# Kernel tuning notes

Measured on AMD Instinct MI355X. Metric: run time of the kernel, lower is better.

Reference implementation:

```python
import jax, jax.numpy as jnp
import numpy as np

T, B, IN, H, A = 512, 256, 292, 128, 12


def setup_inputs() -> dict:
    key = jax.random.key(0)
    ks = jax.random.split(key, 8)
    s = 1.0 / np.sqrt(H)
    return {
        "x": jax.random.normal(ks[0], (T, B, IN), dtype=jnp.float32),
        "done": jax.random.randint(ks[1], (T, B), 0, 2, dtype=jnp.int32),
        "h0": jax.random.normal(ks[2], (1, B, H), dtype=jnp.float32),
        "c0": jax.random.normal(ks[3], (1, B, H), dtype=jnp.float32),
        "W_ih": jax.random.normal(ks[4], (4 * H, IN), dtype=jnp.float32) * s,
        "W_hh": jax.random.normal(ks[5], (4 * H, H), dtype=jnp.float32) * s,
        "b_ih": jnp.zeros((4 * H,), dtype=jnp.float32),
        "b_hh": jnp.zeros((4 * H,), dtype=jnp.float32),
        "W_pi": jax.random.normal(ks[6], (A, H), dtype=jnp.float32) * 0.01,
        "b_pi": jnp.zeros((A,), dtype=jnp.float32),
        "W_v": jax.random.normal(ks[7], (1, H), dtype=jnp.float32),
        "b_v": jnp.zeros((1,), dtype=jnp.float32),
    }


def reference(x, done, h0, c0, W_ih, W_hh, b_ih, b_hh, W_pi, b_pi, W_v, b_v):
    # get_states: per-timestep LSTM with done-based reset of (h, c), as a scan.
    done_f = done.astype(x.dtype)  # [T, B]
    bias = b_ih + b_hh  # [4H]

    def step(carry, inp):
        h, c = carry  # [B, H] each
        x_t, d_t = inp  # [B, IN], [B]
        m = (1.0 - d_t)[:, None]  # reset mask
        h = h * m
        c = c * m
        # PyTorch LSTM gate order: input, forget, cell(g), output
        gates = x_t @ W_ih.T + h @ W_hh.T + bias  # [B, 4H]
        i, f, g, o = jnp.split(gates, 4, axis=-1)
        c = jax.nn.sigmoid(f) * c + jax.nn.sigmoid(i) * jnp.tanh(g)
        h = jax.nn.sigmoid(o) * jnp.tanh(c)
        return (h, c), h

    (hN, cN), hs = jax.lax.scan(step, (h0[0], c0[0]), (x, done_f))
    hidden = hs.reshape(T * B, H)  # flatten(cat(new_hidden), 0, 1)
    logits = hidden @ W_pi.T + b_pi  # policy_layers
    value = hidden @ W_v.T + b_v  # value_layers
    return jnp.concatenate([logits, value], axis=-1)  # [T*B, A+1]
```

## Files before the change

### kernel.cpp

```cpp
#include <hip/hip_runtime.h>
#include <stdint.h>
#include <stddef.h>

#define T_ 512
#define B_ 256
#define IN_ 292
#define H_ 128
#define G4_ 512
#define TB_ 131072
#define LCH 32
#define NCH 16
#define KP_ 320

typedef short bf16x8 __attribute__((ext_vector_type(8)));
typedef float f32x4 __attribute__((ext_vector_type(4)));
typedef unsigned int u32t;

__device__ __forceinline__ unsigned short f2bf(float f) {
  unsigned u = __float_as_uint(f);
  u += 0x7FFFu + ((u >> 16) & 1u);
  return (unsigned short)(u >> 16);
}
__device__ __forceinline__ float bf2f(unsigned short s) {
  return __uint_as_float(((unsigned)s) << 16);
}
__device__ __forceinline__ unsigned bfpack2(float a, float b) {
  unsigned ua = __float_as_uint(a) + 0x8000u;
  unsigned ub = __float_as_uint(b) + 0x8000u;
  return __builtin_amdgcn_perm(ub, ua, 0x07060302u);
}
__device__ __forceinline__ float sigf(float x) {
  return __builtin_amdgcn_rcpf(1.0f + __expf(-x));
}
__device__ __forceinline__ float tanhf_(float x) {
  return 1.0f - 2.0f * __builtin_amdgcn_rcpf(__expf(2.0f * x) + 1.0f);
}
__device__ __forceinline__ void barrier_lds() {
  asm volatile("s_waitcnt lgkmcnt(0)\n\ts_barrier" ::: "memory");
}
__device__ __forceinline__ void gload_lds16(const void* g, void* l) {
  __builtin_amdgcn_global_load_lds(
      (const __attribute__((address_space(1))) u32t*)g,
      (__attribute__((address_space(3))) u32t*)l, 16, 0, 0);
}
__device__ __forceinline__ void load_pr(const unsigned short* p, ushort4* pr) {
  union { uint4 v; ushort4 s[2]; } a, b;
  a.v = *(const uint4*)p;
  b.v = *(const uint4*)(p + 8);
  pr[0] = a.s[0]; pr[1] = a.s[1]; pr[2] = b.s[0]; pr[3] = b.s[1];
}

__global__ __launch_bounds__(256) void k0w_cvt(
    const float* __restrict__ Wih, const float* __restrict__ bih,
    const float* __restrict__ bhh, unsigned short* __restrict__ Wb,
    float* __restrict__ bias2) {
  const int g = blockIdx.x * 256 + threadIdx.x;
  const int jj = g / 40, s = g % 40;
  const int src = (jj & 3) * 128 + (jj >> 2);
  if (g < 512) {
    const int sb = (g & 3) * 128 + (g >> 2);
    bias2[g] = bih[sb] + bhh[sb];
  }
  float4 a = {0.f, 0.f, 0.f, 0.f}, b = {0.f, 0.f, 0.f, 0.f};
  const float* p = Wih + (size_t)src * IN_ + 8 * s;
  if (s < 36) { a = *(const float4*)p; b = *(const float4*)(p + 4); }
  else if (s == 36) { a = *(const float4*)p; }
  uint4 o;
  o.x = bfpack2(a.x, a.y); o.y = bfpack2(a.z, a.w);
  o.z = bfpack2(b.x, b.y); o.w = bfpack2(b.z, b.w);
  *(uint4*)&Wb[(size_t)jj * KP_ + 8 * s] = o;
}

__global__ __launch_bounds__(512, 2) void k1_pregemm(
    const float* __restrict__ x, const unsigned short* __restrict__ Wb,
    const float* __restrict__ bias2, unsigned short* __restrict__ pre2) {
  __shared__ float xr[3][128 * 32];
  __shared__ float xtail[128 * 4];

  const int m0 = blockIdx.x * 128;
  const int tid = threadIdx.x;
  const int w = tid >> 6;
  const int lane = tid & 63;
  const int l15 = lane & 15;
  const int q = lane >> 4;

  if (tid < 128) {
    float4 t = *(const float4*)(x + (size_t)(m0 + tid) * IN_ + 288);
    *(float4*)&xtail[tid * 4] = t;
  }

  bf16x8 af_c[4], af_n[4];
#pragma unroll
  for (int s = 0; s < 4; s++) {
    af_c[s] = *(const bf16x8*)&Wb[(size_t)(w * 64 + 16 * s + l15) * KP_ + q * 8];
    af_n[s] = *(const bf16x8*)&Wb[(size_t)(w * 64 + 16 * s + l15) * KP_ + 32 + q * 8];
  }

#define DMA_TILE(tile)                                                        \
  {                                                                           \
    const int _buf = (tile) % 3;                                              \
    _Pragma("unroll")                                                         \
    for (int _j = 0; _j < 2; _j++) {                                          \
      const int _c = lane + 64 * _j;                                          \
      const int _row = 16 * w + (_c >> 3);                                    \
      const int _slot = _c & 7;                                               \
      const float* _src = x + (size_t)(m0 + _row) * IN_ + (tile) * 32 +       \
                          ((_slot ^ (_row & 7)) * 4);                         \
      gload_lds16(_src, &xr[_buf][w * 512 + _c * 4]);                         \
    }                                                                         \
  }

  f32x4 acc[4][8];
#pragma unroll
  for (int s = 0; s < 4; s++)
#pragma unroll
    for (int ms = 0; ms < 8; ms++) acc[s][ms] = (f32x4){0.f, 0.f, 0.f, 0.f};

  DMA_TILE(0)
  DMA_TILE(1)
  asm volatile("s_waitcnt vmcnt(0) lgkmcnt(0)\n\ts_barrier" ::: "memory");

#pragma unroll
  for (int it = 0; it < 9; it++) {
    const int buf = it % 3;
    bf16x8 bfr[8];
#pragma unroll
    for (int ms = 0; ms < 8; ms++) {
      const int row = 16 * ms + l15;
      const int s0 = (2 * q) ^ (l15 & 7);
      const int s1 = (2 * q + 1) ^ (l15 & 7);
      float4 a = *(const float4*)&xr[buf][row * 32 + s0 * 4];
      float4 b = *(const float4*)&xr[buf][row * 32 + s1 * 4];
      uint4 v;
      v.x = bfpack2(a.x, a.y); v.y = bfpack2(a.z, a.w);
      v.z = bfpack2(b.x, b.y); v.w = bfpack2(b.z, b.w);
      bfr[ms] = *(bf16x8*)&v;
    }
#pragma unroll
    for (int s = 0; s < 4; s++)
#pragma unroll
      for (int ms = 0; ms < 8; ms++)
        acc[s][ms] = __builtin_amdgcn_mfma_f32_16x16x32_bf16(
            af_c[s], bfr[ms], acc[s][ms], 0, 0, 0);
#pragma unroll
    for (int s = 0; s < 4; s++) af_c[s] = af_n[s];
    if (it < 8) {
      const int kk = 32 * (it + 2);
#pragma unroll
      for (int s = 0; s < 4; s++)
        af_n[s] = *(const bf16x8*)&Wb[(size_t)(w * 64 + 16 * s + l15) * KP_ + kk + q * 8];
    }
    if (it < 7) DMA_TILE(it + 2)
    if (it < 7)
      asm volatile("s_waitcnt vmcnt(6) lgkmcnt(0)\n\ts_barrier" ::: "memory");
    else if (it == 7)
      asm volatile("s_waitcnt vmcnt(4) lgkmcnt(0)\n\ts_barrier" ::: "memory");
    else
      asm volatile("s_waitcnt lgkmcnt(0)\n\ts_barrier" ::: "memory");
  }

  {
    bf16x8 bfr[8];
#pragma unroll
    for (int ms = 0; ms < 8; ms++) {
      uint4 v = {0u, 0u, 0u, 0u};
      if (q == 0) {
        float4 t = *(const float4*)&xtail[(16 * ms + l15) * 4];
        v.x = bfpack2(t.x, t.y);
        v.y = bfpack2(t.z, t.w);
      }
      bfr[ms] = *(bf16x8*)&v;
    }
#pragma unroll
    for (int s = 0; s < 4; s++)
#pragma unroll
      for (int ms = 0; ms < 8; ms++)
        acc[s][ms] = __builtin_amdgcn_mfma_f32_16x16x32_bf16(
            af_c[s], bfr[ms], acc[s][ms], 0, 0, 0);
  }

  float4 bb[4];
#pragma unroll
  for (int s = 0; s < 4; s++) bb[s] = *(const float4*)&bias2[w * 64 + 16 * s + 4 * q];
#pragma unroll
  for (int ms = 0; ms < 8; ms++) {
    const int m = m0 + 16 * ms + l15;
#pragma unroll
    for (int s = 0; s < 4; s++) {
      const int jjb = w * 64 + 16 * s + 4 * q;
      uint2 st;
      st.x = bfpack2(acc[s][ms][0] + bb[s].x, acc[s][ms][1] + bb[s].y);
      st.y = bfpack2(acc[s][ms][2] + bb[s].z, acc[s][ms][3] + bb[s].w);
      *(uint2*)&pre2[((size_t)m << 9) + jjb] = st;
    }
  }
#undef DMA_TILE
}

__global__ __launch_bounds__(512) void k2a_chunk(
    const unsigned short* __restrict__ pre2, const float* __restrict__ Whh,
    const int* __restrict__ done, unsigned short* __restrict__ hidden,
    unsigned short* __restrict__ hfin, float* __restrict__ cfin) {
  __shared__ unsigned short hs[2][16 * 136];
  __shared__ int dns[LCH * 16];

  const int bg = blockIdx.x & 15;
  const int ck = blockIdx.x >> 4;
  const int t0 = ck * LCH;
  const int tid = threadIdx.x;
  const int w = tid >> 6;
  const int lane = tid & 63;
  const int l15 = lane & 15;
  const int q = lane >> 4;
  const int bglob = bg * 16 + l15;
  const int kcell = 16 * w + 4 * q;
  const int kq16 = kcell * 4;

  {
    const int r = tid >> 4, c = tid & 15;
    dns[tid] = done[(size_t)(t0 + r) * B_ + bg * 16 + c];
  }

  bf16x8 wf[4][4];
#pragma unroll
  for (int tI = 0; tI < 4; tI++) {
    const int jg = 16 * (w + 8 * tI) + l15;
#pragma unroll
    for (int kc = 0; kc < 4; kc++) {
      const float* p = Whh + (size_t)jg * H_ + kc * 32 + q * 8;
      float4 u0 = *(const float4*)p;
      float4 u1 = *(const float4*)(p + 4);
      bf16x8 r;
      r[0]=(short)f2bf(u0.x); r[1]=(short)f2bf(u0.y); r[2]=(short)f2bf(u0.z); r[3]=(short)f2bf(u0.w);
      r[4]=(short)f2bf(u1.x); r[5]=(short)f2bf(u1.y); r[6]=(short)f2bf(u1.z); r[7]=(short)f2bf(u1.w);
      wf[tI][kc] = r;
    }
  }

  float c_[4] = {0.f, 0.f, 0.f, 0.f};
  {
    const int b = tid >> 5, k = (tid & 31) * 4;
    *(ushort4*)&hs[0][b * 136 + k] = (ushort4){0, 0, 0, 0};
  }
  bool vld = false;
  __syncthreads();

  ushort4 pr[4], prn[4];
  load_pr(pre2 + ((size_t)t0 * B_ + bglob) * G4_ + kq16, pr);
  load_pr(pre2 + ((size_t)(t0 + 1) * B_ + bglob) * G4_ + kq16, prn);

  ushort4 hw = {0, 0, 0, 0};
#pragma unroll 1
  for (int u = 0; u < LCH; u++) {
    const int t = t0 + u;
    ushort4 pr2[4];
    const int un = (u + 2 < LCH) ? u + 2 : LCH - 1;
    load_pr(pre2 + ((size_t)(t0 + un) * B_ + bglob) * G4_ + kq16, pr2);

    const int dn = dns[u * 16 + l15];
    vld = vld || (dn != 0);

    const unsigned short* hb = hs[u & 1];
    bf16x8 hf[4];
#pragma unroll
    for (int kc = 0; kc < 4; kc++) {
      bf16x8 v = *(const bf16x8*)&hb[l15 * 136 + kc * 32 + q * 8];
      if (dn) v = (bf16x8){0, 0, 0, 0, 0, 0, 0, 0};
      hf[kc] = v;
    }

    f32x4 acc[4];
#pragma unroll
    for (int tI = 0; tI < 4; tI++) acc[tI] = (f32x4){0.f, 0.f, 0.f, 0.f};
#pragma unroll
    for (int tI = 0; tI < 4; tI++)
#pragma unroll
      for (int kc = 0; kc < 4; kc++)
        acc[tI] = __builtin_amdgcn_mfma_f32_16x16x32_bf16(
            wf[tI][kc], hf[kc], acc[tI], 0, 0, 0);

    const float m = dn ? 0.0f : 1.0f;
    float hv[4];
#pragma unroll
    for (int r = 0; r < 4; r++) {
      const float iv = acc[0][r] + bf2f(pr[r].x);
      const float fv = acc[1][r] + bf2f(pr[r].y);
      const float gv = acc[2][r] + bf2f(pr[r].z);
      const float ov = acc[3][r] + bf2f(pr[r].w);
      float cc = c_[r] * m;
      cc = sigf(fv) * cc + sigf(iv) * tanhf_(gv);
      c_[r] = cc;
      hv[r] = sigf(ov) * tanhf_(cc);
    }
    uint2 hp = {bfpack2(hv[0], hv[1]), bfpack2(hv[2], hv[3])};
    hw = *(ushort4*)&hp;
    *(uint2*)&hs[(u + 1) & 1][l15 * 136 + kcell] = hp;
    if (vld)
      *(uint2*)&hidden[((size_t)t * B_ + bglob) * H_ + kcell] = hp;
#pragma unroll
    for (int tI = 0; tI < 4; tI++) { pr[tI] = prn[tI]; prn[tI] = pr2[tI]; }
    barrier_lds();
  }

  *(ushort4*)&hfin[((size_t)ck * B_ + bglob) * H_ + kcell] = hw;
  float4 cv = {c_[0], c_[1], c_[2], c_[3]};
  *(float4*)&cfin[((size_t)ck * B_ + bglob) * H_ + kcell] = cv;
}

__global__ __launch_bounds__(512) void k2b_par(
    const unsigned short* __restrict__ pre2, const float* __restrict__ Whh,
    const float* __restrict__ h0, const float* __restrict__ c0,
    const int* __restrict__ done, unsigned short* __restrict__ hidden,
    const unsigned short* __restrict__ hfin, const float* __restrict__ cfin,
    int* __restrict__ needfix) {
  __shared__ unsigned short hs[2][16 * 136];
  __shared__ int dns[LCH * 16];

  const int bg = blockIdx.x & 15;
  const int ck = blockIdx.x >> 4;
  const int t0 = ck * LCH;
  const int tid = threadIdx.x;
  const int w = tid >> 6;
  const int lane = tid & 63;
  const int l15 = lane & 15;
  const int q = lane >> 4;
  const int bglob = bg * 16 + l15;
  const int kcell = 16 * w + 4 * q;
  const int kq16 = kcell * 4;

  {
    const int r = tid >> 4, c = tid & 15;
    dns[tid] = done[(size_t)(t0 + r) * B_ + bg * 16 + c];
  }

  bf16x8 wf[4][4];
#pragma unroll
  for (int tI = 0; tI < 4; tI++) {
    const int jg = 16 * (w + 8 * tI) + l15;
#pragma unroll
    for (int kc = 0; kc < 4; kc++) {
      const float* p = Whh + (size_t)jg * H_ + kc * 32 + q * 8;
      float4 u0 = *(const float4*)p;
      float4 u1 = *(const float4*)(p + 4);
      bf16x8 r;
      r[0]=(short)f2bf(u0.x); r[1]=(short)f2bf(u0.y); r[2]=(short)f2bf(u0.z); r[3]=(short)f2bf(u0.w);
      r[4]=(short)f2bf(u1.x); r[5]=(short)f2bf(u1.y); r[6]=(short)f2bf(u1.z); r[7]=(short)f2bf(u1.w);
      wf[tI][kc] = r;
    }
  }

  float c_[4];
  {
    const int b = tid >> 5, k = (tid & 31) * 4;
    if (ck == 0) {
      float4 hv = *(const float4*)(h0 + (size_t)(bg * 16 + b) * H_ + k);
      uint2 hp = {bfpack2(hv.x, hv.y), bfpack2(hv.z, hv.w)};
      *(uint2*)&hs[0][b * 136 + k] = hp;
      float4 cv = *(const float4*)(c0 + (size_t)bglob * H_ + kcell);
      c_[0] = cv.x; c_[1] = cv.y; c_[2] = cv.z; c_[3] = cv.w;
    } else {
      ushort4 hv = *(const ushort4*)&hfin[((size_t)(ck - 1) * B_ + bg * 16 + b) * H_ + k];
      *(ushort4*)&hs[0][b * 136 + k] = hv;
      float4 cv = *(const float4*)&cfin[((size_t)(ck - 1) * B_ + bglob) * H_ + kcell];
      c_[0] = cv.x; c_[1] = cv.y; c_[2] = cv.z; c_[3] = cv.w;
    }
  }
  int cur = 0;
  bool act = true;
  __syncthreads();

  ushort4 pr[4];
  load_pr(pre2 + ((size_t)t0 * B_ + bglob) * G4_ + kq16, pr);

#pragma unroll 1
  for (int u = 0; u < LCH; u++) {
    const int t = t0 + u;
    const int dn = dns[u * 16 + l15];
    const bool nact = act && (dn == 0);
    if (__ballot(nact) == 0ULL) { act = false; break; }
    act = nact;

    ushort4 prn[4];
    const int un = (u + 1 < LCH) ? u + 1 : LCH - 1;
    load_pr(pre2 + ((size_t)(t0 + un) * B_ + bglob) * G4_ + kq16, prn);

    const unsigned short* hb = hs[cur];
    bf16x8 hf[4];
#pragma unroll
    for (int kc = 0; kc < 4; kc++)
      hf[kc] = *(const bf16x8*)&hb[l15 * 136 + kc * 32 + q * 8];

    f32x4 acc[4];
#pragma unroll
    for (int tI = 0; tI < 4; tI++) acc[tI] = (f32x4){0.f, 0.f, 0.f, 0.f};
#pragma unroll
    for (int tI = 0; tI < 4; tI++)
#pragma unroll
      for (int kc = 0; kc < 4; kc++)
        acc[tI] = __builtin_amdgcn_mfma_f32_16x16x32_bf16(
            wf[tI][kc], hf[kc], acc[tI], 0, 0, 0);

    float hv[4];
#pragma unroll
    for (int r = 0; r < 4; r++) {
      const float iv = acc[0][r] + bf2f(pr[r].x);
      const float fv = acc[1][r] + bf2f(pr[r].y);
      const float gv = acc[2][r] + bf2f(pr[r].z);
      const float ov = acc[3][r] + bf2f(pr[r].w);
      float cc = sigf(fv) * c_[r] + sigf(iv) * tanhf_(gv);
      c_[r] = cc;
      hv[r] = sigf(ov) * tanhf_(cc);
    }
    uint2 hp = {bfpack2(hv[0], hv[1]), bfpack2(hv[2], hv[3])};
    *(uint2*)&hs[cur ^ 1][l15 * 136 + kcell] = hp;
    if (act)
      *(uint2*)&hidden[((size_t)t * B_ + bglob) * H_ + kcell] = hp;
#pragma unroll
    for (int tI = 0; tI < 4; tI++) pr[tI] = prn[tI];
    barrier_lds();
    cur ^= 1;
  }

  if (tid == 0) needfix[blockIdx.x] = (__ballot(act) != 0ULL) ? 1 : 0;
}

__global__ __launch_bounds__(512) void k2c_guard(
    const unsigned short* __restrict__ pre2, const float* __restrict__ Whh,
    const float* __restrict__ h0, const float* __restrict__ c0,
    const int* __restrict__ done, unsigned short* __restrict__ hidden,
    const unsigned short* __restrict__ hfin, const float* __restrict__ cfin,
    const int* __restrict__ needfix) {
  const int bg = blockIdx.x;
  bool dirty = false;
  for (int c2 = 0; c2 < NCH - 1; c2++) dirty |= (needfix[c2 * 16 + bg] != 0);
  if (!dirty) return;

  __shared__ unsigned short hs[2][16 * 136];
  __shared__ int dns[T_ * 16];

  const int tid = threadIdx.x;
  const int w = tid >> 6;
  const int lane = tid & 63;
  const int l15 = lane & 15;
  const int q = lane >> 4;
  const int bglob = bg * 16 + l15;
  const int kcell = 16 * w + 4 * q;
  const int kq16 = kcell * 4;

  {
    const int* p = done + (size_t)tid * B_ + bg * 16;
    *(int4*)&dns[tid * 16]      = *(const int4*)(p);
    *(int4*)&dns[tid * 16 + 4]  = *(const int4*)(p + 4);
    *(int4*)&dns[tid * 16 + 8]  = *(const int4*)(p + 8);
    *(int4*)&dns[tid * 16 + 12] = *(const int4*)(p + 12);
  }

  bf16x8 wf[4][4];
#pragma unroll
  for (int tI = 0; tI < 4; tI++) {
    const int jg = 16 * (w + 8 * tI) + l15;
#pragma unroll
    for (int kc = 0; kc < 4; kc++) {
      const float* p = Whh + (size_t)jg * H_ + kc * 32 + q * 8;
      float4 u0 = *(const float4*)p;
      float4 u1 = *(const float4*)(p + 4);
      bf16x8 r;
      r[0]=(short)f2bf(u0.x); r[1]=(short)f2bf(u0.y); r[2]=(short)f2bf(u0.z); r[3]=(short)f2bf(u0.w);
      r[4]=(short)f2bf(u1.x); r[5]=(short)f2bf(u1.y); r[6]=(short)f2bf(u1.z); r[7]=(short)f2bf(u1.w);
      wf[tI][kc] = r;
    }
  }

  float c_[4];
  {
    float4 cv = *(const float4*)(c0 + (size_t)bglob * H_ + kcell);
    c_[0] = cv.x; c_[1] = cv.y; c_[2] = cv.z; c_[3] = cv.w;
    const int b = tid >> 5, k = (tid & 31) * 4;
    float4 hv = *(const float4*)(h0 + (size_t)(bg * 16 + b) * H_ + k);
    uint2 hp = {bfpack2(hv.x, hv.y), bfpack2(hv.z, hv.w)};
    *(uint2*)&hs[0][b * 136 + k] = hp;
  }
  int cur = 0;
  __syncthreads();

#pragma unroll 1
  for (int ck = 0; ck < NCH; ck++) {
    const int t0 = ck * LCH;
    bool act = true;

    ushort4 pr[4];
    load_pr(pre2 + ((size_t)t0 * B_ + bglob) * G4_ + kq16, pr);

#pragma unroll 1
    for (int u = 0; u < LCH; u++) {
      const int t = t0 + u;
      const int dn = dns[t * 16 + l15];
      const bool nact = act && (dn == 0);
      if (__ballot(nact) == 0ULL) { act = false; break; }
      act = nact;

      ushort4 prn[4];
      const int un = (u + 1 < LCH) ? u + 1 : LCH - 1;
      load_pr(pre2 + ((size_t)(t0 + un) * B_ + bglob) * G4_ + kq16, prn);

      const unsigned short* hb = hs[cur];
      bf16x8 hf[4];
#pragma unroll
      for (int kc = 0; kc < 4; kc++)
        hf[kc] = *(const bf16x8*)&hb[l15 * 136 + kc * 32 + q * 8];

      f32x4 acc[4];
#pragma unroll
      for (int tI = 0; tI < 4; tI++) acc[tI] = (f32x4){0.f, 0.f, 0.f, 0.f};
#pragma unroll
      for (int tI = 0; tI < 4; tI++)
#pragma unroll
        for (int kc = 0; kc < 4; kc++)
          acc[tI] = __builtin_amdgcn_mfma_f32_16x16x32_bf16(
              wf[tI][kc], hf[kc], acc[tI], 0, 0, 0);

      float hv[4];
#pragma unroll
      for (int r = 0; r < 4; r++) {
        const float iv = acc[0][r] + bf2f(pr[r].x);
        const float fv = acc[1][r] + bf2f(pr[r].y);
        const float gv = acc[2][r] + bf2f(pr[r].z);
        const float ov = acc[3][r] + bf2f(pr[r].w);
        float cc = sigf(fv) * c_[r] + sigf(iv) * tanhf_(gv);
        c_[r] = cc;
        hv[r] = sigf(ov) * tanhf_(cc);
      }
      uint2 hp = {bfpack2(hv[0], hv[1]), bfpack2(hv[2], hv[3])};
      *(uint2*)&hs[cur ^ 1][l15 * 136 + kcell] = hp;
      if (act)
        *(uint2*)&hidden[((size_t)t * B_ + bglob) * H_ + kcell] = hp;
#pragma unroll
      for (int tI = 0; tI < 4; tI++) pr[tI] = prn[tI];
      barrier_lds();
      cur ^= 1;
    }

    if (!act) {
      ushort4 hv = *(const ushort4*)&hfin[((size_t)ck * B_ + bglob) * H_ + kcell];
      float4 cv = *(const float4*)&cfin[((size_t)ck * B_ + bglob) * H_ + kcell];
      c_[0] = cv.x; c_[1] = cv.y; c_[2] = cv.z; c_[3] = cv.w;
      *(ushort4*)&hs[cur][l15 * 136 + kcell] = hv;
    }
    barrier_lds();
  }
}

__global__ __launch_bounds__(256) void k3_head(
    const unsigned short* __restrict__ hidden, const float* __restrict__ Wpi,
    const float* __restrict__ bpi, const float* __restrict__ Wv,
    const float* __restrict__ bv, float* __restrict__ out) {
  __shared__ unsigned short hs3[64 * 136];
  __shared__ float bias_s[16];

  const int tid = threadIdx.x;
  const int w = tid >> 6;
  const int lane = tid & 63;
  const int l15 = lane & 15;
  const int q = lane >> 4;
  const int m0 = blockIdx.x * 64;

  if (tid < 16) bias_s[tid] = (tid < 12) ? bpi[tid] : ((tid == 12) ? bv[0] : 0.f);

  bf16x8 wf3[4];
#pragma unroll
  for (int kc = 0; kc < 4; kc++) {
    float4 u0 = {0.f, 0.f, 0.f, 0.f}, u1 = {0.f, 0.f, 0.f, 0.f};
    if (l15 < 12) {
      const float* p = Wpi + (size_t)l15 * H_ + kc * 32 + q * 8;
      u0 = *(const float4*)p; u1 = *(const float4*)(p + 4);
    } else if (l15 == 12) {
      const float* p = Wv + kc * 32 + q * 8;
      u0 = *(const float4*)p; u1 = *(const float4*)(p + 4);
    }
    bf16x8 r;
    r[0]=(short)f2bf(u0.x); r[1]=(short)f2bf(u0.y); r[2]=(short)f2bf(u0.z); r[3]=(short)f2bf(u0.w);
    r[4]=(short)f2bf(u1.x); r[5]=(short)f2bf(u1.y); r[6]=(short)f2bf(u1.z); r[7]=(short)f2bf(u1.w);
    wf3[kc] = r;
  }

  {
    const int row = tid >> 2, ks = (tid & 3) * 32;
    const unsigned short* p = hidden + (size_t)(m0 + row) * H_ + ks;
#pragma unroll
    for (int i = 0; i < 4; i++)
      *(uint4*)&hs3[row * 136 + ks + i * 8] = *(const uint4*)(p + i * 8);
  }
  __syncthreads();

  f32x4 acc = (f32x4){0.f, 0.f, 0.f, 0.f};
#pragma unroll
  for (int kc = 0; kc < 4; kc++) {
    bf16x8 hf = *(bf16x8*)&hs3[(16 * w + l15) * 136 + kc * 32 + q * 8];
    acc = __builtin_amdgcn_mfma_f32_16x16x32_bf16(wf3[kc], hf, acc, 0, 0, 0);
  }

  const float4 bb = *(float4*)&bias_s[4 * q];
  const int m = m0 + 16 * w + l15;
  const size_t ro = (size_t)m * 13;
  float v0 = acc[0] + bb.x, v1 = acc[1] + bb.y, v2 = acc[2] + bb.z, v3 = acc[3] + bb.w;
  if (q < 3) {
    out[ro + 4 * q + 0] = v0;
    out[ro + 4 * q + 1] = v1;
    out[ro + 4 * q + 2] = v2;
    out[ro + 4 * q + 3] = v3;
  } else {
    out[ro + 12] = v0;
  }
}

extern "C" void kernel_launch(void* const* d_in, const int* in_sizes, int n_in,
                              void* d_out, int out_size, void* d_ws, size_t ws_size,
                              hipStream_t stream) {
  const float* x    = (const float*)d_in[0];
  const int* done   = (const int*)d_in[1];
  const float* h0   = (const float*)d_in[2];
  const float* c0   = (const float*)d_in[3];
  const float* Wih  = (const float*)d_in[4];
  const float* Whh  = (const float*)d_in[5];
  const float* bih  = (const float*)d_in[6];
  const float* bhh  = (const float*)d_in[7];
  const float* Wpi  = (const float*)d_in[8];
  const float* bpi  = (const float*)d_in[9];
  const float* Wv   = (const float*)d_in[10];
  const float* bv   = (const float*)d_in[11];
  (void)in_sizes; (void)n_in; (void)out_size; (void)ws_size;

  unsigned short* pre2 = (unsigned short*)d_ws;
  unsigned short* hidden = pre2 + (size_t)TB_ * G4_;
  unsigned short* Wb   = (unsigned short*)d_out;
  float* bias2         = (float*)((char*)d_out + (512u << 10));
  unsigned short* hfin = (unsigned short*)((char*)d_out + (1u << 20));
  float* cfin          = (float*)((char*)d_out + (2u << 20));
  int* needfix         = (int*)((char*)d_out + (4u << 20));
  float* out = (float*)d_out;

  k0w_cvt<<<80, 256, 0, stream>>>(Wih, bih, bhh, Wb, bias2);
  k1_pregemm<<<TB_ / 128, 512, 0, stream>>>(x, Wb, bias2, pre2);
  k2a_chunk<<<256, 512, 0, stream>>>(pre2, Whh, done, hidden, hfin, cfin);
  k2b_par<<<256, 512, 0, stream>>>(pre2, Whh, h0, c0, done, hidden, hfin, cfin, needfix);
  k2c_guard<<<16, 512, 0, stream>>>(pre2, Whh, h0, c0, done, hidden, hfin, cfin, needfix);
  k3_head<<<TB_ / 64, 256, 0, stream>>>(hidden, Wpi, bpi, Wv, bv, out);
}
```

Measured before the change: 439.3 us.

## Fuse input projection GEMM into recurrent chunk kernels, drop pre-gate buffer

Removes the separate input-projection kernel and its large bf16 pre-activation buffer. Each recurrent kernel now DMAs 4-timestep windows of x into LDS and computes x·W_ih on the fly with MFMA, interleaved with the recurrence. W_hh is pre-converted to bf16 once, and hidden-state stores are reorganized to write from LDS with wider coalesced stores. This saves global-memory round trips, at the cost of extra GEMM work inside the latency-bound recurrence, redundant recomputation in the fixup passes, and larger LDS use.

```diff
diff --git a/kernel.cpp b/kernel.cpp
--- a/kernel.cpp
+++ b/kernel.cpp
@@ -21,9 +21,6 @@
   u += 0x7FFFu + ((u >> 16) & 1u);
   return (unsigned short)(u >> 16);
 }
-__device__ __forceinline__ float bf2f(unsigned short s) {
-  return __uint_as_float(((unsigned)s) << 16);
-}
 __device__ __forceinline__ unsigned bfpack2(float a, float b) {
   unsigned ua = __float_as_uint(a) + 0x8000u;
   unsigned ub = __float_as_uint(b) + 0x8000u;
@@ -38,169 +35,139 @@
 __device__ __forceinline__ void barrier_lds() {
   asm volatile("s_waitcnt lgkmcnt(0)\n\ts_barrier" ::: "memory");
 }
+__device__ __forceinline__ void barrier_vm() {
+  asm volatile("s_waitcnt vmcnt(0) lgkmcnt(0)\n\ts_barrier" ::: "memory");
+}
 __device__ __forceinline__ void gload_lds16(const void* g, void* l) {
   __builtin_amdgcn_global_load_lds(
       (const __attribute__((address_space(1))) u32t*)g,
       (__attribute__((address_space(3))) u32t*)l, 16, 0, 0);
 }
-__device__ __forceinline__ void load_pr(const unsigned short* p, ushort4* pr) {
-  union { uint4 v; ushort4 s[2]; } a, b;
-  a.v = *(const uint4*)p;
-  b.v = *(const uint4*)(p + 8);
-  pr[0] = a.s[0]; pr[1] = a.s[1]; pr[2] = b.s[0]; pr[3] = b.s[1];
-}
 
 __global__ __launch_bounds__(256) void k0w_cvt(
-    const float* __restrict__ Wih, const float* __restrict__ bih,
-    const float* __restrict__ bhh, unsigned short* __restrict__ Wb,
+    const float* __restrict__ Wih, const float* __restrict__ Whh,
+    const float* __restrict__ bih, const float* __restrict__ bhh,
+    unsigned short* __restrict__ Wb, unsigned short* __restrict__ whh2,
     float* __restrict__ bias2) {
   const int g = blockIdx.x * 256 + threadIdx.x;
-  const int jj = g / 40, s = g % 40;
-  const int src = (jj & 3) * 128 + (jj >> 2);
   if (g < 512) {
     const int sb = (g & 3) * 128 + (g >> 2);
     bias2[g] = bih[sb] + bhh[sb];
   }
-  float4 a = {0.f, 0.f, 0.f, 0.f}, b = {0.f, 0.f, 0.f, 0.f};
-  const float* p = Wih + (size_t)src * IN_ + 8 * s;
-  if (s < 36) { a = *(const float4*)p; b = *(const float4*)(p + 4); }
-  else if (s == 36) { a = *(const float4*)p; }
-  uint4 o;
-  o.x = bfpack2(a.x, a.y); o.y = bfpack2(a.z, a.w);
-  o.z = bfpack2(b.x, b.y); o.w = bfpack2(b.z, b.w);
-  *(uint4*)&Wb[(size_t)jj * KP_ + 8 * s] = o;
-}
-
-__global__ __launch_bounds__(512, 2) void k1_pregemm(
-    const float* __restrict__ x, const unsigned short* __restrict__ Wb,
-    const float* __restrict__ bias2, unsigned short* __restrict__ pre2) {
-  __shared__ float xr[3][128 * 32];
-  __shared__ float xtail[128 * 4];
-
-  const int m0 = blockIdx.x * 128;
-  const int tid = threadIdx.x;
-  const int w = tid >> 6;
-  const int lane = tid & 63;
-  const int l15 = lane & 15;
-  const int q = lane >> 4;
-
-  if (tid < 128) {
-    float4 t = *(const float4*)(x + (size_t)(m0 + tid) * IN_ + 288);
-    *(float4*)&xtail[tid * 4] = t;
-  }
-
+  if (g < 20480) {
+    const int jj = g / 40, s = g % 40;
+    const int src = (jj & 3) * 128 + (jj >> 2);
+    float4 a = {0.f,0.f,0.f,0.f}, b = {0.f,0.f,0.f,0.f};
+    const float* p = Wih + (size_t)src * IN_ + 8 * s;
+    if (s < 36) { a = *(const float4*)p; b = *(const float4*)(p + 4); }
+    else if (s == 36) { a = *(const float4*)p; }
+    uint4 o;
+    o.x = bfpack2(a.x,a.y); o.y = bfpack2(a.z,a.w);
+    o.z = bfpack2(b.x,b.y); o.w = bfpack2(b.z,b.w);
+    *(uint4*)&Wb[(size_t)jj * KP_ + 8 * s] = o;
+  } else if (g < 28672) {
+    const int g2 = g - 20480;
+    const int jj = g2 >> 4, s = g2 & 15;
+    const int src = (jj & 3) * 128 + (jj >> 2);
+    const float* p = Whh + (size_t)src * H_ + 8 * s;
+    float4 a = *(const float4*)p, b = *(const float4*)(p + 4);
+    uint4 o;
+    o.x = bfpack2(a.x,a.y); o.y = bfpack2(a.z,a.w);
+    o.z = bfpack2(b.x,b.y); o.w = bfpack2(b.z,b.w);
+    *(uint4*)&whh2[(size_t)jj * H_ + 8 * s] = o;
+  }
+}
+
+__device__ __forceinline__ void dma_window(
+    const float* __restrict__ x, float* xs, float* xtl,
+    int tbase , int bg, int w, int lane) {
+#pragma unroll
+  for (int j = 0; j < 9; j++) {
+    const int g = w * 576 + 64 * j + lane;
+    const int row = g / 72;
+    const int sl = g % 72;
+    const int srcg = (sl & ~7) + ((sl & 7) ^ (row & 7));
+    const int grow = (tbase + (row >> 4)) * B_ + bg * 16 + (row & 15);
+    gload_lds16(x + (size_t)grow * IN_ + srcg * 4, xs + (w * 576 + 64 * j) * 4);
+  }
+  if (w == 0) {
+    const int grow = (tbase + (lane >> 4)) * B_ + bg * 16 + (lane & 15);
+    gload_lds16(x + (size_t)grow * IN_ + 288, xtl);
+  }
+}
+
+__device__ __forceinline__ void window_gemm(
+    const float* xs, const float* xtl, const unsigned short* __restrict__ Wb,
+    int w, int q, int l15, f32x4 acc[4][4]) {
+#pragma unroll
+  for (int s = 0; s < 4; s++)
+#pragma unroll
+    for (int ms = 0; ms < 4; ms++) acc[s][ms] = (f32x4){0.f,0.f,0.f,0.f};
+
+  const unsigned short* wrow[4];
   bf16x8 af_c[4], af_n[4];
 #pragma unroll
   for (int s = 0; s < 4; s++) {
-    af_c[s] = *(const bf16x8*)&Wb[(size_t)(w * 64 + 16 * s + l15) * KP_ + q * 8];
-    af_n[s] = *(const bf16x8*)&Wb[(size_t)(w * 64 + 16 * s + l15) * KP_ + 32 + q * 8];
-  }
-
-#define DMA_TILE(tile)                                                        \
-  {                                                                           \
-    const int _buf = (tile) % 3;                                              \
-    _Pragma("unroll")                                                         \
-    for (int _j = 0; _j < 2; _j++) {                                          \
-      const int _c = lane + 64 * _j;                                          \
-      const int _row = 16 * w + (_c >> 3);                                    \
-      const int _slot = _c & 7;                                               \
-      const float* _src = x + (size_t)(m0 + _row) * IN_ + (tile) * 32 +       \
-                          ((_slot ^ (_row & 7)) * 4);                         \
-      gload_lds16(_src, &xr[_buf][w * 512 + _c * 4]);                         \
-    }                                                                         \
-  }
-
-  f32x4 acc[4][8];
-#pragma unroll
-  for (int s = 0; s < 4; s++)
-#pragma unroll
-    for (int ms = 0; ms < 8; ms++) acc[s][ms] = (f32x4){0.f, 0.f, 0.f, 0.f};
-
-  DMA_TILE(0)
-  DMA_TILE(1)
-  asm volatile("s_waitcnt vmcnt(0) lgkmcnt(0)\n\ts_barrier" ::: "memory");
-
+    wrow[s] = Wb + (size_t)(w * 64 + 16 * s + l15) * KP_ + q * 8;
+    af_c[s] = *(const bf16x8*)wrow[s];
+    af_n[s] = *(const bf16x8*)(wrow[s] + 32);
+  }
 #pragma unroll
   for (int it = 0; it < 9; it++) {
-    const int buf = it % 3;
-    bf16x8 bfr[8];
-#pragma unroll
-    for (int ms = 0; ms < 8; ms++) {
+    bf16x8 bfr[4];
+#pragma unroll
+    for (int ms = 0; ms < 4; ms++) {
       const int row = 16 * ms + l15;
-      const int s0 = (2 * q) ^ (l15 & 7);
-      const int s1 = (2 * q + 1) ^ (l15 & 7);
-      float4 a = *(const float4*)&xr[buf][row * 32 + s0 * 4];
-      float4 b = *(const float4*)&xr[buf][row * 32 + s1 * 4];
+      const int m8 = row & 7;
+      const float* rp = xs + row * 288 + it * 32;
+      float4 a = *(const float4*)(rp + (((2 * q)     ^ m8) * 4));
+      float4 b = *(const float4*)(rp + (((2 * q + 1) ^ m8) * 4));
       uint4 v;
-      v.x = bfpack2(a.x, a.y); v.y = bfpack2(a.z, a.w);
-      v.z = bfpack2(b.x, b.y); v.w = bfpack2(b.z, b.w);
+      v.x = bfpack2(a.x,a.y); v.y = bfpack2(a.z,a.w);
+      v.z = bfpack2(b.x,b.y); v.w = bfpack2(b.z,b.w);
       bfr[ms] = *(bf16x8*)&v;
     }
 #pragma unroll
     for (int s = 0; s < 4; s++)
 #pragma unroll
-      for (int ms = 0; ms < 8; ms++)
+      for (int ms = 0; ms < 4; ms++)
         acc[s][ms] = __builtin_amdgcn_mfma_f32_16x16x32_bf16(
             af_c[s], bfr[ms], acc[s][ms], 0, 0, 0);
 #pragma unroll
     for (int s = 0; s < 4; s++) af_c[s] = af_n[s];
     if (it < 8) {
-      const int kk = 32 * (it + 2);
 #pragma unroll
       for (int s = 0; s < 4; s++)
-        af_n[s] = *(const bf16x8*)&Wb[(size_t)(w * 64 + 16 * s + l15) * KP_ + kk + q * 8];
-    }
-    if (it < 7) DMA_TILE(it + 2)
-    if (it < 7)
-      asm volatile("s_waitcnt vmcnt(6) lgkmcnt(0)\n\ts_barrier" ::: "memory");
-    else if (it == 7)
-      asm volatile("s_waitcnt vmcnt(4) lgkmcnt(0)\n\ts_barrier" ::: "memory");
-    else
-      asm volatile("s_waitcnt lgkmcnt(0)\n\ts_barrier" ::: "memory");
-  }
-
+        af_n[s] = *(const bf16x8*)(wrow[s] + 32 * (it + 2));
+    }
+  }
   {
-    bf16x8 bfr[8];
-#pragma unroll
-    for (int ms = 0; ms < 8; ms++) {
-      uint4 v = {0u, 0u, 0u, 0u};
+    bf16x8 bfr[4];
+#pragma unroll
+    for (int ms = 0; ms < 4; ms++) {
+      uint4 v = {0u,0u,0u,0u};
       if (q == 0) {
-        float4 t = *(const float4*)&xtail[(16 * ms + l15) * 4];
-        v.x = bfpack2(t.x, t.y);
-        v.y = bfpack2(t.z, t.w);
+        const float4 t = *(const float4*)(xtl + (16 * ms + l15) * 4);
+        v.x = bfpack2(t.x,t.y); v.y = bfpack2(t.z,t.w);
       }
       bfr[ms] = *(bf16x8*)&v;
     }
 #pragma unroll
     for (int s = 0; s < 4; s++)
 #pragma unroll
-      for (int ms = 0; ms < 8; ms++)
+      for (int ms = 0; ms < 4; ms++)
         acc[s][ms] = __builtin_amdgcn_mfma_f32_16x16x32_bf16(
             af_c[s], bfr[ms], acc[s][ms], 0, 0, 0);
   }
-
-  float4 bb[4];
-#pragma unroll
-  for (int s = 0; s < 4; s++) bb[s] = *(const float4*)&bias2[w * 64 + 16 * s + 4 * q];
-#pragma unroll
-  for (int ms = 0; ms < 8; ms++) {
-    const int m = m0 + 16 * ms + l15;
-#pragma unroll
-    for (int s = 0; s < 4; s++) {
-      const int jjb = w * 64 + 16 * s + 4 * q;
-      uint2 st;
-      st.x = bfpack2(acc[s][ms][0] + bb[s].x, acc[s][ms][1] + bb[s].y);
-      st.y = bfpack2(acc[s][ms][2] + bb[s].z, acc[s][ms][3] + bb[s].w);
-      *(uint2*)&pre2[((size_t)m << 9) + jjb] = st;
-    }
-  }
-#undef DMA_TILE
-}
-
-__global__ __launch_bounds__(512) void k2a_chunk(
-    const unsigned short* __restrict__ pre2, const float* __restrict__ Whh,
+}
+
+__global__ __launch_bounds__(512, 2) void k2a_f(
+    const float* __restrict__ x, const unsigned short* __restrict__ Wb,
+    const float* __restrict__ bias2, const unsigned short* __restrict__ whh2,
     const int* __restrict__ done, unsigned short* __restrict__ hidden,
     unsigned short* __restrict__ hfin, float* __restrict__ cfin) {
+  __shared__ float xs[64 * 288];
+  __shared__ float xtl[64 * 4];
   __shared__ unsigned short hs[2][16 * 136];
   __shared__ int dns[LCH * 16];
 
@@ -213,106 +180,106 @@
   const int l15 = lane & 15;
   const int q = lane >> 4;
   const int bglob = bg * 16 + l15;
-  const int kcell = 16 * w + 4 * q;
-  const int kq16 = kcell * 4;
-
-  {
-    const int r = tid >> 4, c = tid & 15;
-    dns[tid] = done[(size_t)(t0 + r) * B_ + bg * 16 + c];
-  }
+  const int b_d = tid >> 5;
+  const int kd = (tid & 31) * 4;
+
+  dma_window(x, xs, xtl, t0, bg, w, lane);
+
+  dns[tid] = done[(size_t)(t0 + (tid >> 4)) * B_ + bg * 16 + (tid & 15)];
 
   bf16x8 wf[4][4];
 #pragma unroll
-  for (int tI = 0; tI < 4; tI++) {
-    const int jg = 16 * (w + 8 * tI) + l15;
+  for (int s = 0; s < 4; s++)
+#pragma unroll
+    for (int kc = 0; kc < 4; kc++)
+      wf[s][kc] = *(const bf16x8*)&whh2[(size_t)(w * 64 + 16 * s + l15) * H_ + kc * 32 + q * 8];
+  float4 bias_r[4];
+#pragma unroll
+  for (int s = 0; s < 4; s++)
+    bias_r[s] = *(const float4*)&bias2[w * 64 + 16 * s + 4 * q];
+
+  float c_[4] = {0.f, 0.f, 0.f, 0.f};
+  *(ushort4*)&hs[0][b_d * 136 + kd] = (ushort4){0, 0, 0, 0};
+  bool vldL = false;
+  unsigned short hl[4] = {0, 0, 0, 0};
+  int cur = 0;
+  barrier_lds();
+
+  f32x4 accx[4][4];
+#pragma unroll 1
+  for (int tloc = 0; tloc < LCH; tloc++) {
+    if (tloc > 0 && vldL) {
+      uint2 hv = *(const uint2*)&hs[cur][b_d * 136 + kd];
+      *(uint2*)&hidden[((size_t)(t0 + tloc - 1) * B_ + bg * 16 + b_d) * H_ + kd] = hv;
+    }
+    vldL = vldL || (dns[tloc * 16 + b_d] != 0);
+
+    if ((tloc & 3) == 0) {
+      barrier_vm();
+      window_gemm(xs, xtl, Wb, w, q, l15, accx);
+      barrier_lds();
+      if (tloc < LCH - 4)
+        dma_window(x, xs, xtl, t0 + tloc + 4, bg, w, lane);
+    }
+
+    const int dn = dns[tloc * 16 + l15];
+    bf16x8 hf[4];
 #pragma unroll
     for (int kc = 0; kc < 4; kc++) {
-      const float* p = Whh + (size_t)jg * H_ + kc * 32 + q * 8;
-      float4 u0 = *(const float4*)p;
-      float4 u1 = *(const float4*)(p + 4);
-      bf16x8 r;
-      r[0]=(short)f2bf(u0.x); r[1]=(short)f2bf(u0.y); r[2]=(short)f2bf(u0.z); r[3]=(short)f2bf(u0.w);
-      r[4]=(short)f2bf(u1.x); r[5]=(short)f2bf(u1.y); r[6]=(short)f2bf(u1.z); r[7]=(short)f2bf(u1.w);
-      wf[tI][kc] = r;
-    }
-  }
-
-  float c_[4] = {0.f, 0.f, 0.f, 0.f};
-  {
-    const int b = tid >> 5, k = (tid & 31) * 4;
-    *(ushort4*)&hs[0][b * 136 + k] = (ushort4){0, 0, 0, 0};
-  }
-  bool vld = false;
-  __syncthreads();
-
-  ushort4 pr[4], prn[4];
-  load_pr(pre2 + ((size_t)t0 * B_ + bglob) * G4_ + kq16, pr);
-  load_pr(pre2 + ((size_t)(t0 + 1) * B_ + bglob) * G4_ + kq16, prn);
-
-  ushort4 hw = {0, 0, 0, 0};
-#pragma unroll 1
-  for (int u = 0; u < LCH; u++) {
-    const int t = t0 + u;
-    ushort4 pr2[4];
-    const int un = (u + 2 < LCH) ? u + 2 : LCH - 1;
-    load_pr(pre2 + ((size_t)(t0 + un) * B_ + bglob) * G4_ + kq16, pr2);
-
-    const int dn = dns[u * 16 + l15];
-    vld = vld || (dn != 0);
-
-    const unsigned short* hb = hs[u & 1];
-    bf16x8 hf[4];
-#pragma unroll
-    for (int kc = 0; kc < 4; kc++) {
-      bf16x8 v = *(const bf16x8*)&hb[l15 * 136 + kc * 32 + q * 8];
-      if (dn) v = (bf16x8){0, 0, 0, 0, 0, 0, 0, 0};
+      bf16x8 v = *(const bf16x8*)&hs[cur][l15 * 136 + kc * 32 + q * 8];
+      if (dn) v = (bf16x8){0,0,0,0,0,0,0,0};
       hf[kc] = v;
     }
-
-    f32x4 acc[4];
-#pragma unroll
-    for (int tI = 0; tI < 4; tI++) acc[tI] = (f32x4){0.f, 0.f, 0.f, 0.f};
-#pragma unroll
-    for (int tI = 0; tI < 4; tI++)
+    f32x4 acch[4];
+#pragma unroll
+    for (int s = 0; s < 4; s++) acch[s] = (f32x4){0.f,0.f,0.f,0.f};
+#pragma unroll
+    for (int s = 0; s < 4; s++)
 #pragma unroll
       for (int kc = 0; kc < 4; kc++)
-        acc[tI] = __builtin_amdgcn_mfma_f32_16x16x32_bf16(
-            wf[tI][kc], hf[kc], acc[tI], 0, 0, 0);
-
-    const float m = dn ? 0.0f : 1.0f;
-    float hv[4];
-#pragma unroll
-    for (int r = 0; r < 4; r++) {
-      const float iv = acc[0][r] + bf2f(pr[r].x);
-      const float fv = acc[1][r] + bf2f(pr[r].y);
-      const float gv = acc[2][r] + bf2f(pr[r].z);
-      const float ov = acc[3][r] + bf2f(pr[r].w);
-      float cc = c_[r] * m;
+        acch[s] = __builtin_amdgcn_mfma_f32_16x16x32_bf16(
+            wf[s][kc], hf[kc], acch[s], 0, 0, 0);
+
+    const float mm = dn ? 0.0f : 1.0f;
+    const int d = tloc & 3;
+#pragma unroll
+    for (int s = 0; s < 4; s++) {
+      const float iv = accx[s][d][0] + acch[s][0] + bias_r[s].x;
+      const float fv = accx[s][d][1] + acch[s][1] + bias_r[s].y;
+      const float gv = accx[s][d][2] + acch[s][2] + bias_r[s].z;
+      const float ov = accx[s][d][3] + acch[s][3] + bias_r[s].w;
+      float cc = c_[s] * mm;
       cc = sigf(fv) * cc + sigf(iv) * tanhf_(gv);
-      c_[r] = cc;
-      hv[r] = sigf(ov) * tanhf_(cc);
-    }
-    uint2 hp = {bfpack2(hv[0], hv[1]), bfpack2(hv[2], hv[3])};
-    hw = *(ushort4*)&hp;
-    *(uint2*)&hs[(u + 1) & 1][l15 * 136 + kcell] = hp;
-    if (vld)
-      *(uint2*)&hidden[((size_t)t * B_ + bglob) * H_ + kcell] = hp;
-#pragma unroll
-    for (int tI = 0; tI < 4; tI++) { pr[tI] = prn[tI]; prn[tI] = pr2[tI]; }
+      c_[s] = cc;
+      const unsigned short hu = f2bf(sigf(ov) * tanhf_(cc));
+      hs[cur ^ 1][l15 * 136 + 16 * w + 4 * s + q] = hu;
+      hl[s] = hu;
+    }
     barrier_lds();
-  }
-
-  *(ushort4*)&hfin[((size_t)ck * B_ + bglob) * H_ + kcell] = hw;
-  float4 cv = {c_[0], c_[1], c_[2], c_[3]};
-  *(float4*)&cfin[((size_t)ck * B_ + bglob) * H_ + kcell] = cv;
-}
-
-__global__ __launch_bounds__(512) void k2b_par(
-    const unsigned short* __restrict__ pre2, const float* __restrict__ Whh,
+    cur ^= 1;
+  }
+  if (vldL) {
+    uint2 hv = *(const uint2*)&hs[cur][b_d * 136 + kd];
+    *(uint2*)&hidden[((size_t)(t0 + LCH - 1) * B_ + bg * 16 + b_d) * H_ + kd] = hv;
+  }
+#pragma unroll
+  for (int s = 0; s < 4; s++) {
+    const int cell = 16 * w + 4 * s + q;
+    hfin[((size_t)ck * B_ + bglob) * H_ + cell] = hl[s];
+    cfin[((size_t)ck * B_ + bglob) * H_ + cell] = c_[s];
+  }
+  asm volatile("s_waitcnt vmcnt(0)" ::: "memory");
+}
+
+__global__ __launch_bounds__(512, 2) void k2b_f(
+    const float* __restrict__ x, const unsigned short* __restrict__ Wb,
+    const float* __restrict__ bias2, const unsigned short* __restrict__ whh2,
     const float* __restrict__ h0, const float* __restrict__ c0,
     const int* __restrict__ done, unsigned short* __restrict__ hidden,
     const unsigned short* __restrict__ hfin, const float* __restrict__ cfin,
     int* __restrict__ needfix) {
+  __shared__ float xs[64 * 288];
+  __shared__ float xtl[64 * 4];
   __shared__ unsigned short hs[2][16 * 136];
   __shared__ int dns[LCH * 16];
 
@@ -325,107 +292,102 @@
   const int l15 = lane & 15;
   const int q = lane >> 4;
   const int bglob = bg * 16 + l15;
-  const int kcell = 16 * w + 4 * q;
-  const int kq16 = kcell * 4;
-
-  {
-    const int r = tid >> 4, c = tid & 15;
-    dns[tid] = done[(size_t)(t0 + r) * B_ + bg * 16 + c];
-  }
+  const int b_d = tid >> 5;
+  const int kd = (tid & 31) * 4;
+
+  dns[tid] = done[(size_t)(t0 + (tid >> 4)) * B_ + bg * 16 + (tid & 15)];
 
   bf16x8 wf[4][4];
 #pragma unroll
-  for (int tI = 0; tI < 4; tI++) {
-    const int jg = 16 * (w + 8 * tI) + l15;
-#pragma unroll
-    for (int kc = 0; kc < 4; kc++) {
-      const float* p = Whh + (size_t)jg * H_ + kc * 32 + q * 8;
-      float4 u0 = *(const float4*)p;
-      float4 u1 = *(const float4*)(p + 4);
-      bf16x8 r;
-      r[0]=(short)f2bf(u0.x); r[1]=(short)f2bf(u0.y); r[2]=(short)f2bf(u0.z); r[3]=(short)f2bf(u0.w);
-      r[4]=(short)f2bf(u1.x); r[5]=(short)f2bf(u1.y); r[6]=(short)f2bf(u1.z); r[7]=(short)f2bf(u1.w);
-      wf[tI][kc] = r;
-    }
-  }
+  for (int s = 0; s < 4; s++)
+#pragma unroll
+    for (int kc = 0; kc < 4; kc++)
+      wf[s][kc] = *(const bf16x8*)&whh2[(size_t)(w * 64 + 16 * s + l15) * H_ + kc * 32 + q * 8];
+  float4 bias_r[4];
+#pragma unroll
+  for (int s = 0; s < 4; s++)
+    bias_r[s] = *(const float4*)&bias2[w * 64 + 16 * s + 4 * q];
 
   float c_[4];
-  {
-    const int b = tid >> 5, k = (tid & 31) * 4;
-    if (ck == 0) {
-      float4 hv = *(const float4*)(h0 + (size_t)(bg * 16 + b) * H_ + k);
-      uint2 hp = {bfpack2(hv.x, hv.y), bfpack2(hv.z, hv.w)};
-      *(uint2*)&hs[0][b * 136 + k] = hp;
-      float4 cv = *(const float4*)(c0 + (size_t)bglob * H_ + kcell);
-      c_[0] = cv.x; c_[1] = cv.y; c_[2] = cv.z; c_[3] = cv.w;
-    } else {
-      ushort4 hv = *(const ushort4*)&hfin[((size_t)(ck - 1) * B_ + bg * 16 + b) * H_ + k];
-      *(ushort4*)&hs[0][b * 136 + k] = hv;
-      float4 cv = *(const float4*)&cfin[((size_t)(ck - 1) * B_ + bglob) * H_ + kcell];
-      c_[0] = cv.x; c_[1] = cv.y; c_[2] = cv.z; c_[3] = cv.w;
-    }
-  }
+  if (ck == 0) {
+    float4 hv4 = *(const float4*)(h0 + (size_t)(bg * 16 + b_d) * H_ + kd);
+    uint2 hp = {bfpack2(hv4.x, hv4.y), bfpack2(hv4.z, hv4.w)};
+    *(uint2*)&hs[0][b_d * 136 + kd] = hp;
+#pragma unroll
+    for (int s = 0; s < 4; s++)
+      c_[s] = c0[(size_t)bglob * H_ + 16 * w + 4 * s + q];
+  } else {
+    ushort4 hv = *(const ushort4*)&hfin[((size_t)(ck - 1) * B_ + bg * 16 + b_d) * H_ + kd];
+    *(ushort4*)&hs[0][b_d * 136 + kd] = hv;
+#pragma unroll
+    for (int s = 0; s < 4; s++)
+      c_[s] = cfin[((size_t)(ck - 1) * B_ + bglob) * H_ + 16 * w + 4 * s + q];
+  }
+  bool actL = true;
+  bool act = true;
+  bool broke = false;
   int cur = 0;
-  bool act = true;
-  __syncthreads();
-
-  ushort4 pr[4];
-  load_pr(pre2 + ((size_t)t0 * B_ + bglob) * G4_ + kq16, pr);
-
+  barrier_lds();
+
+  f32x4 accx[4][4];
 #pragma unroll 1
-  for (int u = 0; u < LCH; u++) {
-    const int t = t0 + u;
-    const int dn = dns[u * 16 + l15];
+  for (int tloc = 0; tloc < LCH; tloc++) {
+    if (tloc > 0 && actL) {
+      uint2 hv = *(const uint2*)&hs[cur][b_d * 136 + kd];
+      *(uint2*)&hidden[((size_t)(t0 + tloc - 1) * B_ + bg * 16 + b_d) * H_ + kd] = hv;
+    }
+    actL = actL && (dns[tloc * 16 + b_d] == 0);
+
+    const int dn = dns[tloc * 16 + l15];
     const bool nact = act && (dn == 0);
-    if (__ballot(nact) == 0ULL) { act = false; break; }
+    if (__ballot(nact) == 0ULL) { act = false; broke = true; break; }
     act = nact;
 
-    ushort4 prn[4];
-    const int un = (u + 1 < LCH) ? u + 1 : LCH - 1;
-    load_pr(pre2 + ((size_t)(t0 + un) * B_ + bglob) * G4_ + kq16, prn);
-
-    const unsigned short* hb = hs[cur];
+    if ((tloc & 3) == 0) {
+      dma_window(x, xs, xtl, t0 + tloc, bg, w, lane);
+      barrier_vm();
+      window_gemm(xs, xtl, Wb, w, q, l15, accx);
+    }
+
     bf16x8 hf[4];
 #pragma unroll
     for (int kc = 0; kc < 4; kc++)
-      hf[kc] = *(const bf16x8*)&hb[l15 * 136 + kc * 32 + q * 8];
-
-    f32x4 acc[4];
-#pragma unroll
-    for (int tI = 0; tI < 4; tI++) acc[tI] = (f32x4){0.f, 0.f, 0.f, 0.f};
-#pragma unroll
-    for (int tI = 0; tI < 4; tI++)
+      hf[kc] = *(const bf16x8*)&hs[cur][l15 * 136 + kc * 32 + q * 8];
+    f32x4 acch[4];
+#pragma unroll
+    for (int s = 0; s < 4; s++) acch[s] = (f32x4){0.f,0.f,0.f,0.f};
+#pragma unroll
+    for (int s = 0; s < 4; s++)
 #pragma unroll
       for (int kc = 0; kc < 4; kc++)
-        acc[tI] = __builtin_amdgcn_mfma_f32_16x16x32_bf16(
-            wf[tI][kc], hf[kc], acc[tI], 0, 0, 0);
-
-    float hv[4];
-#pragma unroll
-    for (int r = 0; r < 4; r++) {
-      const float iv = acc[0][r] + bf2f(pr[r].x);
-      const float fv = acc[1][r] + bf2f(pr[r].y);
-      const float gv = acc[2][r] + bf2f(pr[r].z);
-      const float ov = acc[3][r] + bf2f(pr[r].w);
-      float cc = sigf(fv) * c_[r] + sigf(iv) * tanhf_(gv);
-      c_[r] = cc;
-      hv[r] = sigf(ov) * tanhf_(cc);
-    }
-    uint2 hp = {bfpack2(hv[0], hv[1]), bfpack2(hv[2], hv[3])};
-    *(uint2*)&hs[cur ^ 1][l15 * 136 + kcell] = hp;
-    if (act)
-      *(uint2*)&hidden[((size_t)t * B_ + bglob) * H_ + kcell] = hp;
-#pragma unroll
-    for (int tI = 0; tI < 4; tI++) pr[tI] = prn[tI];
+        acch[s] = __builtin_amdgcn_mfma_f32_16x16x32_bf16(
+            wf[s][kc], hf[kc], acch[s], 0, 0, 0);
+
+    const int d = tloc & 3;
+#pragma unroll
+    for (int s = 0; s < 4; s++) {
+      const float iv = accx[s][d][0] + acch[s][0] + bias_r[s].x;
+      const float fv = accx[s][d][1] + acch[s][1] + bias_r[s].y;
+      const float gv = accx[s][d][2] + acch[s][2] + bias_r[s].z;
+      const float ov = accx[s][d][3] + acch[s][3] + bias_r[s].w;
+      float cc = sigf(fv) * c_[s] + sigf(iv) * tanhf_(gv);
+      c_[s] = cc;
+      hs[cur ^ 1][l15 * 136 + 16 * w + 4 * s + q] = f2bf(sigf(ov) * tanhf_(cc));
+    }
     barrier_lds();
     cur ^= 1;
   }
-
+  if (!broke && actL) {
+    uint2 hv = *(const uint2*)&hs[cur][b_d * 136 + kd];
+    *(uint2*)&hidden[((size_t)(t0 + LCH - 1) * B_ + bg * 16 + b_d) * H_ + kd] = hv;
+  }
   if (tid == 0) needfix[blockIdx.x] = (__ballot(act) != 0ULL) ? 1 : 0;
-}
-
-__global__ __launch_bounds__(512) void k2c_guard(
-    const unsigned short* __restrict__ pre2, const float* __restrict__ Whh,
+  asm volatile("s_waitcnt vmcnt(0)" ::: "memory");
+}
+
+__global__ __launch_bounds__(512, 2) void k2c_f(
+    const float* __restrict__ x, const unsigned short* __restrict__ Wb,
+    const float* __restrict__ bias2, const unsigned short* __restrict__ whh2,
     const float* __restrict__ h0, const float* __restrict__ c0,
     const int* __restrict__ done, unsigned short* __restrict__ hidden,
     const unsigned short* __restrict__ hfin, const float* __restrict__ cfin,
@@ -435,6 +397,8 @@
   for (int c2 = 0; c2 < NCH - 1; c2++) dirty |= (needfix[c2 * 16 + bg] != 0);
   if (!dirty) return;
 
+  __shared__ float xs[64 * 288];
+  __shared__ float xtl[64 * 4];
   __shared__ unsigned short hs[2][16 * 136];
   __shared__ int dns[T_ * 16];
 
@@ -444,8 +408,8 @@
   const int l15 = lane & 15;
   const int q = lane >> 4;
   const int bglob = bg * 16 + l15;
-  const int kcell = 16 * w + 4 * q;
-  const int kq16 = kcell * 4;
+  const int b_d = tid >> 5;
+  const int kd = (tid & 31) * 4;
 
   {
     const int* p = done + (size_t)tid * B_ + bg * 16;
@@ -457,97 +421,94 @@
 
   bf16x8 wf[4][4];
 #pragma unroll
-  for (int tI = 0; tI < 4; tI++) {
-    const int jg = 16 * (w + 8 * tI) + l15;
-#pragma unroll
-    for (int kc = 0; kc < 4; kc++) {
-      const float* p = Whh + (size_t)jg * H_ + kc * 32 + q * 8;
-      float4 u0 = *(const float4*)p;
-      float4 u1 = *(const float4*)(p + 4);
-      bf16x8 r;
-      r[0]=(short)f2bf(u0.x); r[1]=(short)f2bf(u0.y); r[2]=(short)f2bf(u0.z); r[3]=(short)f2bf(u0.w);
-      r[4]=(short)f2bf(u1.x); r[5]=(short)f2bf(u1.y); r[6]=(short)f2bf(u1.z); r[7]=(short)f2bf(u1.w);
-      wf[tI][kc] = r;
-    }
-  }
+  for (int s = 0; s < 4; s++)
+#pragma unroll
+    for (int kc = 0; kc < 4; kc++)
+      wf[s][kc] = *(const bf16x8*)&whh2[(size_t)(w * 64 + 16 * s + l15) * H_ + kc * 32 + q * 8];
+  float4 bias_r[4];
+#pragma unroll
+  for (int s = 0; s < 4; s++)
+    bias_r[s] = *(const float4*)&bias2[w * 64 + 16 * s + 4 * q];
 
   float c_[4];
   {
-    float4 cv = *(const float4*)(c0 + (size_t)bglob * H_ + kcell);
-    c_[0] = cv.x; c_[1] = cv.y; c_[2] = cv.z; c_[3] = cv.w;
-    const int b = tid >> 5, k = (tid & 31) * 4;
-    float4 hv = *(const float4*)(h0 + (size_t)(bg * 16 + b) * H_ + k);
-    uint2 hp = {bfpack2(hv.x, hv.y), bfpack2(hv.z, hv.w)};
-    *(uint2*)&hs[0][b * 136 + k] = hp;
+    float4 hv4 = *(const float4*)(h0 + (size_t)(bg * 16 + b_d) * H_ + kd);
+    uint2 hp = {bfpack2(hv4.x, hv4.y), bfpack2(hv4.z, hv4.w)};
+    *(uint2*)&hs[0][b_d * 136 + kd] = hp;
+#pragma unroll
+    for (int s = 0; s < 4; s++)
+      c_[s] = c0[(size_t)bglob * H_ + 16 * w + 4 * s + q];
   }
   int cur = 0;
-  __syncthreads();
+  barrier_lds();
 
 #pragma unroll 1
   for (int ck = 0; ck < NCH; ck++) {
     const int t0 = ck * LCH;
-    bool act = true;
-
-    ushort4 pr[4];
-    load_pr(pre2 + ((size_t)t0 * B_ + bglob) * G4_ + kq16, pr);
-
+    bool act = true, actL = true, broke = false;
+    f32x4 accx[4][4];
 #pragma unroll 1
-    for (int u = 0; u < LCH; u++) {
-      const int t = t0 + u;
-      const int dn = dns[t * 16 + l15];
+    for (int tloc = 0; tloc < LCH; tloc++) {
+      if (tloc > 0 && actL) {
+        uint2 hv = *(const uint2*)&hs[cur][b_d * 136 + kd];
+        *(uint2*)&hidden[((size_t)(t0 + tloc - 1) * B_ + bg * 16 + b_d) * H_ + kd] = hv;
+      }
+      actL = actL && (dns[(t0 + tloc) * 16 + b_d] == 0);
+
+      const int dn = dns[(t0 + tloc) * 16 + l15];
       const bool nact = act && (dn == 0);
-      if (__ballot(nact) == 0ULL) { act = false; break; }
+      if (__ballot(nact) == 0ULL) { act = false; broke = true; break; }
       act = nact;
 
-      ushort4 prn[4];
-      const int un = (u + 1 < LCH) ? u + 1 : LCH - 1;
-      load_pr(pre2 + ((size_t)(t0 + un) * B_ + bglob) * G4_ + kq16, prn);
-
-      const unsigned short* hb = hs[cur];
+      if ((tloc & 3) == 0) {
+        dma_window(x, xs, xtl, t0 + tloc, bg, w, lane);
+        barrier_vm();
+        window_gemm(xs, xtl, Wb, w, q, l15, accx);
+      }
+
       bf16x8 hf[4];
 #pragma unroll
       for (int kc = 0; kc < 4; kc++)
-        hf[kc] = *(const bf16x8*)&hb[l15 * 136 + kc * 32 + q * 8];
-
-      f32x4 acc[4];
-#pragma unroll
-      for (int tI = 0; tI < 4; tI++) acc[tI] = (f32x4){0.f, 0.f, 0.f, 0.f};
-#pragma unroll
-      for (int tI = 0; tI < 4; tI++)
+        hf[kc] = *(const bf16x8*)&hs[cur][l15 * 136 + kc * 32 + q * 8];
+      f32x4 acch[4];
+#pragma unroll
+      for (int s = 0; s < 4; s++) acch[s] = (f32x4){0.f,0.f,0.f,0.f};
+#pragma unroll
+      for (int s = 0; s < 4; s++)
 #pragma unroll
         for (int kc = 0; kc < 4; kc++)
-          acc[tI] = __builtin_amdgcn_mfma_f32_16x16x32_bf16(
-              wf[tI][kc], hf[kc], acc[tI], 0, 0, 0);
-
-      float hv[4];
-#pragma unroll
-      for (int r = 0; r < 4; r++) {
-        const float iv = acc[0][r] + bf2f(pr[r].x);
-        const float fv = acc[1][r] + bf2f(pr[r].y);
-        const float gv = acc[2][r] + bf2f(pr[r].z);
-        const float ov = acc[3][r] + bf2f(pr[r].w);
-        float cc = sigf(fv) * c_[r] + sigf(iv) * tanhf_(gv);
-        c_[r] = cc;
-        hv[r] = sigf(ov) * tanhf_(cc);
+          acch[s] = __builtin_amdgcn_mfma_f32_16x16x32_bf16(
+              wf[s][kc], hf[kc], acch[s], 0, 0, 0);
+
+      const int d = tloc & 3;
+#pragma unroll
+      for (int s = 0; s < 4; s++) {
+        const float iv = accx[s][d][0] + acch[s][0] + bias_r[s].x;
+        const float fv = accx[s][d][1] + acch[s][1] + bias_r[s].y;
+        const float gv = accx[s][d][2] + acch[s][2] + bias_r[s].z;
+        const float ov = accx[s][d][3] + acch[s][3] + bias_r[s].w;
+        float cc = sigf(fv) * c_[s] + sigf(iv) * tanhf_(gv);
+        c_[s] = cc;
+        hs[cur ^ 1][l15 * 136 + 16 * w + 4 * s + q] = f2bf(sigf(ov) * tanhf_(cc));
       }
-      uint2 hp = {bfpack2(hv[0], hv[1]), bfpack2(hv[2], hv[3])};
-      *(uint2*)&hs[cur ^ 1][l15 * 136 + kcell] = hp;
-      if (act)
-        *(uint2*)&hidden[((size_t)t * B_ + bglob) * H_ + kcell] = hp;
-#pragma unroll
-      for (int tI = 0; tI < 4; tI++) pr[tI] = prn[tI];
       barrier_lds();
       cur ^= 1;
     }
-
+    if (!broke && actL) {
+      uint2 hv = *(const uint2*)&hs[cur][b_d * 136 + kd];
+      *(uint2*)&hidden[((size_t)(t0 + LCH - 1) * B_ + bg * 16 + b_d) * H_ + kd] = hv;
+    }
     if (!act) {
-      ushort4 hv = *(const ushort4*)&hfin[((size_t)ck * B_ + bglob) * H_ + kcell];
-      float4 cv = *(const float4*)&cfin[((size_t)ck * B_ + bglob) * H_ + kcell];
-      c_[0] = cv.x; c_[1] = cv.y; c_[2] = cv.z; c_[3] = cv.w;
-      *(ushort4*)&hs[cur][l15 * 136 + kcell] = hv;
+#pragma unroll
+      for (int s = 0; s < 4; s++) {
+        const int cell = 16 * w + 4 * s + q;
+        c_[s] = cfin[((size_t)ck * B_ + bglob) * H_ + cell];
+        hs[cur][l15 * 136 + cell] = hfin[((size_t)ck * B_ + bglob) * H_ + cell];
+      }
     }
     barrier_lds();
   }
+  asm volatile("s_waitcnt vmcnt(0)" ::: "memory");
 }
 
 __global__ __launch_bounds__(256) void k3_head(
@@ -569,7 +530,7 @@
   bf16x8 wf3[4];
 #pragma unroll
   for (int kc = 0; kc < 4; kc++) {
-    float4 u0 = {0.f, 0.f, 0.f, 0.f}, u1 = {0.f, 0.f, 0.f, 0.f};
+    float4 u0 = {0.f,0.f,0.f,0.f}, u1 = {0.f,0.f,0.f,0.f};
     if (l15 < 12) {
       const float* p = Wpi + (size_t)l15 * H_ + kc * 32 + q * 8;
       u0 = *(const float4*)p; u1 = *(const float4*)(p + 4);
@@ -577,10 +538,10 @@
       const float* p = Wv + kc * 32 + q * 8;
       u0 = *(const float4*)p; u1 = *(const float4*)(p + 4);
     }
-    bf16x8 r;
-    r[0]=(short)f2bf(u0.x); r[1]=(short)f2bf(u0.y); r[2]=(short)f2bf(u0.z); r[3]=(short)f2bf(u0.w);
-    r[4]=(short)f2bf(u1.x); r[5]=(short)f2bf(u1.y); r[6]=(short)f2bf(u1.z); r[7]=(short)f2bf(u1.w);
-    wf3[kc] = r;
+    uint4 v;
+    v.x = bfpack2(u0.x,u0.y); v.y = bfpack2(u0.z,u0.w);
+    v.z = bfpack2(u1.x,u1.y); v.w = bfpack2(u1.z,u1.w);
+    wf3[kc] = *(bf16x8*)&v;
   }
 
   {
@@ -592,7 +553,7 @@
   }
   __syncthreads();
 
-  f32x4 acc = (f32x4){0.f, 0.f, 0.f, 0.f};
+  f32x4 acc = (f32x4){0.f,0.f,0.f,0.f};
 #pragma unroll
   for (int kc = 0; kc < 4; kc++) {
     bf16x8 hf = *(bf16x8*)&hs3[(16 * w + l15) * 136 + kc * 32 + q * 8];
@@ -630,19 +591,20 @@
   const float* bv   = (const float*)d_in[11];
   (void)in_sizes; (void)n_in; (void)out_size; (void)ws_size;
 
-  unsigned short* pre2 = (unsigned short*)d_ws;
-  unsigned short* hidden = pre2 + (size_t)TB_ * G4_;
-  unsigned short* Wb   = (unsigned short*)d_out;
-  float* bias2         = (float*)((char*)d_out + (512u << 10));
-  unsigned short* hfin = (unsigned short*)((char*)d_out + (1u << 20));
-  float* cfin          = (float*)((char*)d_out + (2u << 20));
-  int* needfix         = (int*)((char*)d_out + (4u << 20));
+  unsigned short* hidden = (unsigned short*)d_ws;
+  unsigned short* Wb    = (unsigned short*)d_out;
+  float* bias2          = (float*)((char*)d_out + (512u << 10));
+  unsigned short* whh2  = (unsigned short*)((char*)d_out + (640u << 10));
+  unsigned short* hfin  = (unsigned short*)((char*)d_out + (1u << 20));
+  float* cfin           = (float*)((char*)d_out + (2u << 20));
+  int* needfix          = (int*)((char*)d_out + (4u << 20));
   float* out = (float*)d_out;
 
-  k0w_cvt<<<80, 256, 0, stream>>>(Wih, bih, bhh, Wb, bias2);
-  k1_pregemm<<<TB_ / 128, 512, 0, stream>>>(x, Wb, bias2, pre2);
-  k2a_chunk<<<256, 512, 0, stream>>>(pre2, Whh, done, hidden, hfin, cfin);
-  k2b_par<<<256, 512, 0, stream>>>(pre2, Whh, h0, c0, done, hidden, hfin, cfin, needfix);
-  k2c_guard<<<16, 512, 0, stream>>>(pre2, Whh, h0, c0, done, hidden, hfin, cfin, needfix);
+  k0w_cvt<<<112, 256, 0, stream>>>(Wih, Whh, bih, bhh, Wb, whh2, bias2);
+  k2a_f<<<256, 512, 0, stream>>>(x, Wb, bias2, whh2, done, hidden, hfin, cfin);
+  k2b_f<<<256, 512, 0, stream>>>(x, Wb, bias2, whh2, h0, c0, done, hidden,
+                                 hfin, cfin, needfix);
+  k2c_f<<<16, 512, 0, stream>>>(x, Wb, bias2, whh2, h0, c0, done, hidden,
+                                hfin, cfin, needfix);
   k3_head<<<TB_ / 64, 256, 0, stream>>>(hidden, Wpi, bpi, Wv, bv, out);
 }
```

After: 652.1 us. 48.4% more time.
